# Performance work log

Hardware: AMD Instinct MI355X
Metric: run time of the kernel (lower is better)

## Reference

```python
import jax, jax.numpy as jnp
import numpy as np

B, N, BQ, BK = 2, 2048, 32, 128
NB = N // BQ
CS, CZ, CH, H, PQK, PV = 384, 128, 16, 12, 4, 8
INF, EPS = 1e5, 1e-8
CONCAT = CZ // 4 + CH + PV * 4  # per-head concat feature dim


def _ln(x, g, b):
    m = jnp.mean(x, -1, keepdims=True)
    v = jnp.mean((x - m) ** 2, -1, keepdims=True)
    return (x - m) * jax.lax.rsqrt(v + 1e-5) * g + b


def _forward(s, z, trans, rots, s_mask, key_idx,
             ln_s_g, ln_s_b, ln_z_g, ln_z_b,
             Wq, Wk, Wv, Wqp, Wkvp, Wb, Wdz, head_weights, Wout):
    sN = _ln(s, ln_s_g, ln_s_b)                     # [B,N,CS]
    zN = _ln(z, ln_z_g, ln_z_b)                     # [B,NB,BQ,BK,CZ]
    q_in = sN.reshape(B, NB, BQ, CS)                # to_queries = block reshape
    k_in = sN[:, key_idx]                           # to_keys = gather [B,NB,BK,CS]
    q_t = trans.reshape(B, NB, BQ, 3)
    q_R = rots.reshape(B, NB, BQ, 3, 3)
    k_t = trans[:, key_idx]                         # [B,NB,BK,3]
    k_R = rots[:, key_idx]                          # [B,NB,BK,3,3]

    q = (q_in @ Wq).reshape(B, NB, BQ, H, CH)
    k = (k_in @ Wk).reshape(B, NB, BK, H, CH)
    v = (k_in @ Wv).reshape(B, NB, BK, H, CH)

    # query points: local -> global frame (R p + t)
    q_pts = (q_in @ Wqp).reshape(B, NB, BQ, H * PQK, 3)
    q_pts = jnp.einsum('bnqij,bnqpj->bnqpi', q_R, q_pts) + q_t[..., None, :]
    q_pts = q_pts.reshape(B, NB, BQ, H, PQK, 3)
    kv_pts = (k_in @ Wkvp).reshape(B, NB, BK, H * (PQK + PV), 3)
    kv_pts = jnp.einsum('bnkij,bnkpj->bnkpi', k_R, kv_pts) + k_t[..., None, :]
    kv_pts = kv_pts.reshape(B, NB, BK, H, PQK + PV, 3)
    k_pts, v_pts = kv_pts[..., :PQK, :], kv_pts[..., PQK:, :]

    bbias = zN @ Wb                                 # [B,NB,BQ,BK,H]
    a = jnp.einsum('bnqhc,bnkhc->bnqkh', q, k) * np.float32(np.sqrt(1.0 / (3 * CH)))
    a = a + np.float32(np.sqrt(1.0 / 3)) * bbias

    # point-distance bias (pts_cdist=True path)
    pt = -2.0 * jnp.einsum('bnqhpd,bnkhpd->bnqkh', q_pts, k_pts)
    qn = jnp.sum(q_pts ** 2, axis=(-1, -2))         # [B,NB,BQ,H]
    kn = jnp.sum(k_pts ** 2, axis=(-1, -2))         # [B,NB,BK,H]
    pt = pt + qn[..., None, :] + kn[..., None, :, :]
    hw = jax.nn.softplus(head_weights) * np.float32(np.sqrt(1.0 / (3 * (PQK * 9.0 / 2))))
    pt = pt * hw * (-0.5)
    a = a + pt

    q_mask = s_mask.reshape(B, NB, BQ)
    k_mask = s_mask[:, key_idx]                     # [B,NB,BK]
    am = q_mask[..., :, None] * k_mask[..., None, :]  # [B,NB,BQ,BK]
    a = a + (INF * (am - 1.0))[..., None]
    a = jnp.swapaxes(a, -1, -2)                     # [B,NB,BQ,H,BK]
    a = jax.nn.softmax(a, axis=-1)

    o = jnp.einsum('bnqhk,bnkhc->bnqhc', a, v).reshape(B, NB, BQ, H * CH)
    o_pt = jnp.einsum('bnqhk,bnkhvc->bnqhvc', a, v_pts)   # [B,NB,BQ,H,PV,3]
    # invert apply: R^T (p - t), back into the query local frame
    o_pt = jnp.einsum('bnqji,bnqhvj->bnqhvi', q_R, o_pt - q_t[..., None, None, :])
    o_pt_d = jnp.sqrt(jnp.sum(o_pt ** 2, -1) + EPS).reshape(B, NB, BQ, H * PV)
    o_pt_f = o_pt.reshape(B, NB, BQ, H * PV * 3)
    pair_z = zN @ Wdz                               # [B,NB,BQ,BK,CZ//4]
    o_pair = jnp.einsum('bnqhk,bnqkc->bnqhc', a, pair_z).reshape(B, NB, BQ, H * (CZ // 4))

    feats = jnp.concatenate([o, o_pt_f, o_pt_d, o_pair], -1)  # [B,NB,BQ,H*CONCAT]
    out = feats @ Wout
    return out.reshape(B, N, CS)


def setup_inputs() -> dict:
    key = jax.random.key(0)
    ks = jax.random.split(key, 16)
    def p(i, shape, scale):
        return jax.random.normal(ks[i], shape, jnp.float32) * scale
    s = p(0, (B, N, CS), 1.0)
    z = p(1, (B, NB, BQ, BK, CZ), 1.0)
    trans = p(2, (B, N, 3), 1.0)
    rots = p(3, (B, N, 3, 3), 1.0)
    s_mask = jnp.ones((B, N), jnp.float32)
    starts = np.clip(np.arange(NB) * BQ - (BK - BQ) // 2, 0, N - BK)
    key_idx = jnp.asarray(starts[:, None] + np.arange(BK)[None, :], jnp.int32)
    return dict(
        s=s, z=z, trans=trans, rots=rots, s_mask=s_mask, key_idx=key_idx,
        ln_s_g=jnp.ones((CS,), jnp.float32), ln_s_b=jnp.zeros((CS,), jnp.float32),
        ln_z_g=jnp.ones((CZ,), jnp.float32), ln_z_b=jnp.zeros((CZ,), jnp.float32),
        Wq=p(4, (CS, H * CH), CS ** -0.5), Wk=p(5, (CS, H * CH), CS ** -0.5),
        Wv=p(6, (CS, H * CH), CS ** -0.5),
        Wqp=p(7, (CS, H * PQK * 3), CS ** -0.5),
        Wkvp=p(8, (CS, H * (PQK + PV) * 3), CS ** -0.5),
        Wb=p(9, (CZ, H), CZ ** -0.5), Wdz=p(10, (CZ, CZ // 4), CZ ** -0.5),
        head_weights=p(11, (H,), 0.5),
        Wout=p(12, (H * CONCAT, CS), 0.02),
    )


def reference(s, z, trans, rots, s_mask, key_idx,
              ln_s_g, ln_s_b, ln_z_g, ln_z_b,
              Wq, Wk, Wv, Wqp, Wkvp, Wb, Wdz, head_weights, Wout):
    return _forward(s, z, trans, rots, s_mask, key_idx,
                    ln_s_g, ln_s_b, ln_z_g, ln_z_b,
                    Wq, Wk, Wv, Wqp, Wkvp, Wb, Wdz, head_weights, Wout)
```

## Files before the change

kernel.cpp:

```cpp
#include <hip/hip_runtime.h>
#include <hip/hip_bf16.h>


typedef unsigned int uint_t;
typedef unsigned short ushort_t;
__device__ __forceinline__ float b2f(const __hip_bfloat16 x) { return __bfloat162float(x); }
__device__ __forceinline__ __hip_bfloat16 f2b(float x) { return __float2bfloat16(x); }
__device__ __forceinline__ ushort_t f2bu(float x) {
  __hip_bfloat16 h = __float2bfloat16(x);
  return *(ushort_t*)&h;
}
__device__ __forceinline__ float b2fu(ushort_t u) {
  union { uint_t i; float f; } c; c.i = ((uint_t)u) << 16; return c.f;
}
__device__ __forceinline__ uint_t pack2(float a, float b) {
  return (uint_t)f2bu(a) | ((uint_t)f2bu(b) << 16);
}
typedef __attribute__((ext_vector_type(8))) short short8x;
typedef __attribute__((ext_vector_type(4))) float floatx4;

__global__ __launch_bounds__(256) void k_ln(
    const float* __restrict__ s, const float* __restrict__ g_s,
    const float* __restrict__ b_s, float* __restrict__ sN,
    const float* __restrict__ g_z, const float* __restrict__ b_z,
    const float* __restrict__ Wb, const float* __restrict__ Wdz,
    ushort_t* __restrict__ Wt_g, float* __restrict__ uv_g)
{
  if (blockIdx.x >= 512) {
    const int tid = threadIdx.x;
    for (int e = tid; e < 48 * 128; e += 256) {
      int c = e >> 7, k = e & 127;
      float v = 0.f;
      if (c < 12)      v = g_z[k] * Wb[k * 12 + c];
      else if (c < 44) v = g_z[k] * Wdz[k * 32 + (c - 12)];
      Wt_g[e] = f2bu(v);
    }
    int c = tid >> 2, p = tid & 3;
    float us_ = 0.f, vs_ = 0.f;
    if (c < 44) {
      for (int k = p * 32; k < p * 32 + 32; k++) {
        float worig = (c < 12) ? Wb[k * 12 + c] : Wdz[k * 32 + (c - 12)];
        us_ += b2fu(f2bu(g_z[k] * worig));
        vs_ += b_z[k] * worig;
      }
    }
    us_ += __shfl_xor(us_, 1, 64); us_ += __shfl_xor(us_, 2, 64);
    vs_ += __shfl_xor(vs_, 1, 64); vs_ += __shfl_xor(vs_, 2, 64);
    if (p == 0 && c < 48) { uv_g[c] = us_; uv_g[48 + c] = vs_; }
    return;
  }
  const int tid = threadIdx.x;
  const int w = tid >> 6, l = tid & 63;
  #pragma unroll
  for (int ii = 0; ii < 2; ii++) {
    int row = blockIdx.x * 8 + w * 2 + ii;
    const float* sr = s + (size_t)row * 384;
    float x[6], s1 = 0.f, s2 = 0.f;
    #pragma unroll
    for (int j = 0; j < 6; j++) { x[j] = sr[l + j * 64]; s1 += x[j]; s2 += x[j] * x[j]; }
    #pragma unroll
    for (int m = 1; m < 64; m <<= 1) { s1 += __shfl_xor(s1, m, 64); s2 += __shfl_xor(s2, m, 64); }
    float mean = s1 * (1.f / 384.f);
    float var = s2 * (1.f / 384.f) - mean * mean;
    float rstd = rsqrtf(var + 1e-5f);
    float* dr = sN + (size_t)row * 384;
    #pragma unroll
    for (int j = 0; j < 6; j++) {
      int c = l + j * 64;
      dr[c] = (x[j] - mean) * rstd * g_s[c] + b_s[c];
    }
  }
}

__global__ __launch_bounds__(256) void k_zpg(
    const float* __restrict__ sN,
    const float* __restrict__ Wq, const float* __restrict__ Wk,
    const float* __restrict__ Wv, const float* __restrict__ Wqp,
    const float* __restrict__ Wkvp,
    float* __restrict__ proj,
    const float* __restrict__ z,
    const ushort_t* __restrict__ Wt_g, const float* __restrict__ uv_g,
    ushort_t* __restrict__ bbias_t, ushort_t* __restrict__ pzt)
{
  if (blockIdx.x < 1152) {
    __shared__ __align__(16) float sA[16][32];
    __shared__ __align__(16) float sB[16][128];
    const int tid = threadIdx.x;
    const int bid = blockIdx.x;
    const int mt = bid & 127;
    const int nt = bid >> 7;
    const int m0 = mt * 32, n0 = nt * 128;
    const int tm = tid >> 5, tn = tid & 31;

    const float* bsrc[2]; int bstride[2]; int bk[2];
    #pragma unroll
    for (int u = 0; u < 2; u++) {
      int idx = tid + u * 256;
      int k = idx >> 5, n4 = idx & 31;
      int col0 = n0 + n4 * 4;
      const float* p; int st;
      if (col0 < 192)      { p = Wq   + col0;         st = 192; }
      else if (col0 < 384) { p = Wk   + (col0 - 192); st = 192; }
      else if (col0 < 576) { p = Wv   + (col0 - 384); st = 192; }
      else if (col0 < 720) { p = Wqp  + (col0 - 576); st = 144; }
      else                 { p = Wkvp + (col0 - 720); st = 432; }
      bsrc[u] = p; bstride[u] = st; bk[u] = k;
    }
    const int am = tid >> 2, ak4 = tid & 3;

    float acc[4][4];
    #pragma unroll
    for (int i = 0; i < 4; i++)
      #pragma unroll
      for (int j = 0; j < 4; j++) acc[i][j] = 0.f;

    for (int k0 = 0; k0 < 384; k0 += 16) {
      #pragma unroll
      for (int u = 0; u < 2; u++) {
        float4 wv4 = *(const float4*)(bsrc[u] + (size_t)(k0 + bk[u]) * bstride[u]);
        *(float4*)&sB[bk[u]][(tid + u * 256 & 31) * 4] = wv4;
      }
      if (tid < 128) {
        float4 a4 = *(const float4*)(sN + (size_t)(m0 + am) * 384 + k0 + ak4 * 4);
        sA[ak4 * 4 + 0][am] = a4.x;
        sA[ak4 * 4 + 1][am] = a4.y;
        sA[ak4 * 4 + 2][am] = a4.z;
        sA[ak4 * 4 + 3][am] = a4.w;
      }
      __syncthreads();
      #pragma unroll
      for (int kk = 0; kk < 16; kk++) {
        float4 a4 = *(const float4*)&sA[kk][tm * 4];
        float4 b4 = *(const float4*)&sB[kk][tn * 4];
        const float* av = (const float*)&a4;
        const float* bv = (const float*)&b4;
        #pragma unroll
        for (int i = 0; i < 4; i++)
          #pragma unroll
          for (int j = 0; j < 4; j++) acc[i][j] += av[i] * bv[j];
      }
      __syncthreads();
    }
    #pragma unroll
    for (int i = 0; i < 4; i++)
      *(float4*)(proj + (size_t)(m0 + tm * 4 + i) * 1152 + n0 + tn * 4) = *(float4*)&acc[i][0];
  } else {
    const int tid = threadIdx.x;
    const int bid = blockIdx.x - 1152;
    const int w = tid >> 6, lane = tid & 63, quad = lane >> 4, r16 = lane & 15;
    const size_t row0 = (size_t)bid * 64;
    const int lrow = w * 16 + r16;
    const float* zr = z + (row0 + lrow) * 128;

    short8x bf[3][4];
    #pragma unroll
    for (int nt = 0; nt < 3; nt++)
      #pragma unroll
      for (int kk = 0; kk < 4; kk++)
        bf[nt][kk] = *(const short8x*)(Wt_g + (size_t)(nt * 16 + r16) * 128 + kk * 32 + quad * 8);

    union { short8x v; uint_t u[4]; } afu[4];
    float s1 = 0.f, s2 = 0.f;
    #pragma unroll
    for (int kk = 0; kk < 4; kk++) {
      float4 a = *(const float4*)(zr + kk * 32 + quad * 8);
      float4 b = *(const float4*)(zr + kk * 32 + quad * 8 + 4);
      s1 += a.x + a.y + a.z + a.w + b.x + b.y + b.z + b.w;
      s2 += a.x * a.x + a.y * a.y + a.z * a.z + a.w * a.w
          + b.x * b.x + b.y * b.y + b.z * b.z + b.w * b.w;
      afu[kk].u[0] = pack2(a.x, a.y);
      afu[kk].u[1] = pack2(a.z, a.w);
      afu[kk].u[2] = pack2(b.x, b.y);
      afu[kk].u[3] = pack2(b.z, b.w);
    }
    s1 += __shfl_xor(s1, 16, 64); s1 += __shfl_xor(s1, 32, 64);
    s2 += __shfl_xor(s2, 16, 64); s2 += __shfl_xor(s2, 32, 64);
    float mean = s1 * (1.f / 128.f);
    float rstd = rsqrtf(s2 * (1.f / 128.f) - mean * mean + 1e-5f);

    floatx4 acc[3] = { {0,0,0,0}, {0,0,0,0}, {0,0,0,0} };
    #pragma unroll
    for (int kk = 0; kk < 4; kk++)
      #pragma unroll
      for (int nt = 0; nt < 3; nt++)
        acc[nt] = __builtin_amdgcn_mfma_f32_16x16x32_bf16(afu[kk].v, bf[nt][kk], acc[nt], 0, 0, 0);

    float mr[4], rr[4];
    #pragma unroll
    for (int reg = 0; reg < 4; reg++) {
      int src = quad * 4 + reg;
      mr[reg] = __shfl(mean, src, 64);
      rr[reg] = __shfl(rstd, src, 64);
    }

    const int bp = bid >> 6;
    const int qk0 = (bid & 63) * 64;
    const int qloc = qk0 >> 7;
    const int kbase = (qk0 & 127) + w * 16 + quad * 4;
    #pragma unroll
    for (int nt = 0; nt < 3; nt++) {
      int c = nt * 16 + r16;
      if (c < 44) {
        float uc = uv_g[c], vc = uv_g[48 + c];
        float vals[4];
        #pragma unroll
        for (int reg = 0; reg < 4; reg++)
          vals[reg] = rr[reg] * acc[nt][reg] - mr[reg] * rr[reg] * uc + vc;
        uint2 pk = make_uint2(pack2(vals[0], vals[1]), pack2(vals[2], vals[3]));
        if (c < 12) {
          size_t el = (((size_t)(bp * 12 + c)) << 12) + qk0 + w * 16 + quad * 4;
          *(uint2*)(bbias_t + el) = pk;
        } else {
          size_t el = (((size_t)((bp * 32 + qloc) * 32 + (c - 12))) << 7) + kbase;
          *(uint2*)(pzt + el) = pk;
        }
      }
    }
  }
}

__global__ __launch_bounds__(256) void k_rot(
    const float* __restrict__ proj_g,
    const float* __restrict__ trans, const float* __restrict__ rots,
    float* __restrict__ posq, float* __restrict__ posk, float* __restrict__ posv,
    float* __restrict__ posqp, float* __restrict__ poskp, float* __restrict__ posvp,
    float* __restrict__ posqn, float* __restrict__ poskn)
{
  __shared__ __align__(16) float proj[8][1152];
  __shared__ float rt[8][12];
  const int tid = threadIdx.x;
  const int p0 = blockIdx.x * 8;

  for (int e = tid; e < 8 * 288; e += 256)
    ((float4*)&proj[0][0])[e] = ((const float4*)(proj_g + (size_t)p0 * 1152))[e];
  for (int e = tid; e < 8 * 12; e += 256) {
    int i = e / 12, c = e % 12;
    rt[i][c] = (c < 9) ? rots[(size_t)(p0 + i) * 9 + c]
                       : trans[(size_t)(p0 + i) * 3 + (c - 9)];
  }
  __syncthreads();

  for (int e = tid; e < 8 * 192; e += 256) {
    int i = e / 192, p = e % 192;
    float R0 = rt[i][0], R1 = rt[i][1], R2 = rt[i][2];
    float R3 = rt[i][3], R4 = rt[i][4], R5 = rt[i][5];
    float R6 = rt[i][6], R7 = rt[i][7], R8 = rt[i][8];
    float tx = rt[i][9], ty = rt[i][10], tz = rt[i][11];
    size_t pos = p0 + i;
    if (p < 48) {
      int base = 576 + p * 3;
      float v0 = proj[i][base], v1 = proj[i][base + 1], v2 = proj[i][base + 2];
      float o0 = R0 * v0 + R1 * v1 + R2 * v2 + tx;
      float o1 = R3 * v0 + R4 * v1 + R5 * v2 + ty;
      float o2 = R6 * v0 + R7 * v1 + R8 * v2 + tz;
      proj[i][base] = o0; proj[i][base + 1] = o1; proj[i][base + 2] = o2;
      posqp[pos * 144 + p * 3 + 0] = o0;
      posqp[pos * 144 + p * 3 + 1] = o1;
      posqp[pos * 144 + p * 3 + 2] = o2;
    } else {
      int p2 = p - 48;
      int base = 720 + p2 * 3;
      float v0 = proj[i][base], v1 = proj[i][base + 1], v2 = proj[i][base + 2];
      float o0 = R0 * v0 + R1 * v1 + R2 * v2 + tx;
      float o1 = R3 * v0 + R4 * v1 + R5 * v2 + ty;
      float o2 = R6 * v0 + R7 * v1 + R8 * v2 + tz;
      int h = p2 / 12, idx = p2 % 12;
      if (idx < 4) {
        proj[i][base] = o0; proj[i][base + 1] = o1; proj[i][base + 2] = o2;
        poskp[pos * 144 + h * 12 + idx * 3 + 0] = o0;
        poskp[pos * 144 + h * 12 + idx * 3 + 1] = o1;
        poskp[pos * 144 + h * 12 + idx * 3 + 2] = o2;
      } else {
        posvp[pos * 288 + h * 24 + (idx - 4) * 3 + 0] = o0;
        posvp[pos * 288 + h * 24 + (idx - 4) * 3 + 1] = o1;
        posvp[pos * 288 + h * 24 + (idx - 4) * 3 + 2] = o2;
      }
    }
  }
  __syncthreads();

  for (int e = tid; e < 96; e += 256) {
    int i = e / 12, h = e % 12;
    size_t pos = p0 + i;
    float qs = 0.f, ks = 0.f;
    #pragma unroll
    for (int u = 0; u < 12; u++) {
      float a_ = proj[i][576 + h * 12 + u];
      qs += a_ * a_;
      float c_ = proj[i][720 + h * 36 + u];
      ks += c_ * c_;
    }
    posqn[pos * 12 + h] = qs;
    poskn[pos * 12 + h] = ks;
  }
  for (int e = tid; e < 8 * 576; e += 256) {
    int i = e / 576, c = e % 576;
    size_t pos = p0 + i;
    float v = proj[i][c];
    if (c < 192)      posq[pos * 192 + c]         = v;
    else if (c < 384) posk[pos * 192 + (c - 192)] = v;
    else              posv[pos * 192 + (c - 384)] = v;
  }
}

__global__ __launch_bounds__(256) void k_attn(
    const float* __restrict__ posq, const float* __restrict__ posk,
    const float* __restrict__ posv, const float* __restrict__ posqp,
    const float* __restrict__ poskp, const float* __restrict__ posvp,
    const float* __restrict__ posqn, const float* __restrict__ poskn,
    const ushort_t* __restrict__ bbias_t,
    const float* __restrict__ s_mask, const int* __restrict__ key_idx,
    const float* __restrict__ trans, const float* __restrict__ rots,
    const float* __restrict__ head_w,
    float* __restrict__ feats, ushort_t* __restrict__ P_ws)
{
  __shared__ __align__(16) ushort_t sK[2 * 128 * 40];
  __shared__ __align__(16) ushort_t sV[2 * 48 * 136];
  __shared__ __align__(16) ushort_t sQ[2 * 32 * 40];
  __shared__ __align__(16) ushort_t sP[64 * 136];
  __shared__ float sOpt[64 * 25];
  __shared__ float rt[32][12];
  __shared__ float kn_l[2][128];
  __shared__ float qn_l[2][32];
  __shared__ float kmask[128];
  __shared__ float qmask[32];
  __shared__ int   kidx[128];
  __shared__ float hwe2[2];

  const int tid = threadIdx.x;
  const int bid = blockIdx.x;
  const int b = bid / 384;
  const int rem = bid % 384;
  const int nb = rem / 6;
  const int hp = rem % 6;
  const int h0 = hp * 2;
  const int rowbase = b * 2048 + nb * 32;

  if (tid < 128) kidx[tid] = key_idx[nb * 128 + tid];
  if (tid < 2) hwe2[tid] = -0.5f * 0.13608276348795434f * log1pf(expf(head_w[h0 + tid]));
  __syncthreads();

  if (tid < 128) kmask[tid] = s_mask[b * 2048 + kidx[tid]];
  if (tid < 32) qmask[tid] = s_mask[rowbase + tid];
  for (int e = tid; e < 384; e += 256) {
    int i = e / 12, c = e % 12;
    rt[i][c] = (c < 9) ? rots[(size_t)(rowbase + i) * 9 + c]
                       : trans[(size_t)(rowbase + i) * 3 + (c - 9)];
  }

  {
    int hh = tid >> 7, k = tid & 127, h = h0 + hh;
    int gk = b * 2048 + kidx[k];
    kn_l[hh][k] = poskn[(size_t)gk * 12 + h];
    float sq = 0.14433756729740643f;
    float sp = -2.f * hwe2[hh];
    const float* kr = posk + (size_t)gk * 192 + h * 16;
    #pragma unroll
    for (int c4 = 0; c4 < 4; c4++) {
      float4 v4 = *(const float4*)(kr + c4 * 4);
      uint2 pk = make_uint2(pack2(sq * v4.x, sq * v4.y), pack2(sq * v4.z, sq * v4.w));
      *(uint2*)&sK[(hh * 128 + k) * 40 + c4 * 4] = pk;
    }
    const float* kpr = poskp + (size_t)gk * 144 + h * 12;
    #pragma unroll
    for (int c4 = 0; c4 < 3; c4++) {
      float4 v4 = *(const float4*)(kpr + c4 * 4);
      uint2 pk = make_uint2(pack2(sp * v4.x, sp * v4.y), pack2(sp * v4.z, sp * v4.w));
      *(uint2*)&sK[(hh * 128 + k) * 40 + 16 + c4 * 4] = pk;
    }
    *(uint2*)&sK[(hh * 128 + k) * 40 + 28] = make_uint2(0u, 0u);
  }
  {
    int hh = tid >> 7, t7 = tid & 127, h = h0 + hh;
    int k2 = t7 >> 1, cg = t7 & 1, kk0 = k2 * 2;
    int ga = b * 2048 + kidx[kk0], gb = b * 2048 + kidx[kk0 + 1];
    if (cg == 0) {
      const float* A_ = posv + (size_t)ga * 192 + h * 16;
      const float* B_ = posv + (size_t)gb * 192 + h * 16;
      #pragma unroll
      for (int c4 = 0; c4 < 4; c4++) {
        float4 a4 = *(const float4*)(A_ + c4 * 4);
        float4 b4 = *(const float4*)(B_ + c4 * 4);
        #pragma unroll
        for (int j = 0; j < 4; j++)
          *(uint_t*)&sV[(hh * 48 + c4 * 4 + j) * 136 + kk0] =
              pack2(((const float*)&a4)[j], ((const float*)&b4)[j]);
      }
    } else {
      const float* A_ = posvp + (size_t)ga * 288 + h * 24;
      const float* B_ = posvp + (size_t)gb * 288 + h * 24;
      #pragma unroll
      for (int c4 = 0; c4 < 6; c4++) {
        float4 a4 = *(const float4*)(A_ + c4 * 4);
        float4 b4 = *(const float4*)(B_ + c4 * 4);
        #pragma unroll
        for (int j = 0; j < 4; j++)
          *(uint_t*)&sV[(hh * 48 + 16 + c4 * 4 + j) * 136 + kk0] =
              pack2(((const float*)&a4)[j], ((const float*)&b4)[j]);
      }
      #pragma unroll
      for (int j = 0; j < 8; j++)
        *(uint_t*)&sV[(hh * 48 + 40 + j) * 136 + kk0] = 0u;
    }
  }
  if (tid < 64) {
    int hh = tid >> 5, q = tid & 31, h = h0 + hh;
    qn_l[hh][q] = posqn[(size_t)(rowbase + q) * 12 + h];
    const float* qr = posq + (size_t)(rowbase + q) * 192 + h * 16;
    #pragma unroll
    for (int c4 = 0; c4 < 4; c4++) {
      float4 v4 = *(const float4*)(qr + c4 * 4);
      uint2 pk = make_uint2(pack2(v4.x, v4.y), pack2(v4.z, v4.w));
      *(uint2*)&sQ[(hh * 32 + q) * 40 + c4 * 4] = pk;
    }
    const float* qpr = posqp + (size_t)(rowbase + q) * 144 + h * 12;
    #pragma unroll
    for (int c4 = 0; c4 < 3; c4++) {
      float4 v4 = *(const float4*)(qpr + c4 * 4);
      uint2 pk = make_uint2(pack2(v4.x, v4.y), pack2(v4.z, v4.w));
      *(uint2*)&sQ[(hh * 32 + q) * 40 + 16 + c4 * 4] = pk;
    }
    *(uint2*)&sQ[(hh * 32 + q) * 40 + 28] = make_uint2(0u, 0u);
  }
  __syncthreads();

  const int w = tid >> 6, lane = tid & 63, quad = lane >> 4, r16 = lane & 15;
  const int hh = w >> 1, q0 = (w & 1) * 16;
  const int h = h0 + hh;
  const float hwe = hwe2[hh];

  short8x af = *(const short8x*)&sQ[(hh * 32 + q0 + r16) * 40 + quad * 8];
  floatx4 acc[8];
  #pragma unroll
  for (int nt = 0; nt < 8; nt++) {
    floatx4 z4 = {0.f, 0.f, 0.f, 0.f};
    short8x bf = *(const short8x*)&sK[(hh * 128 + nt * 16 + r16) * 40 + quad * 8];
    acc[nt] = __builtin_amdgcn_mfma_f32_16x16x32_bf16(af, bf, z4, 0, 0, 0);
  }

  const ushort_t* bb = bbias_t + (((size_t)((b * 64 + nb) * 12 + h)) << 12);
  float lg[8][4];
  #pragma unroll
  for (int nt = 0; nt < 8; nt++)
    #pragma unroll
    for (int reg = 0; reg < 4; reg++) {
      int qa = q0 + quad * 4 + reg;
      lg[nt][reg] = b2fu(bb[qa * 128 + nt * 16 + r16]);
    }
  float qnv[4], qmv[4];
  #pragma unroll
  for (int reg = 0; reg < 4; reg++) {
    int qa = q0 + quad * 4 + reg;
    qnv[reg] = qn_l[hh][qa]; qmv[reg] = qmask[qa];
  }
  #pragma unroll
  for (int nt = 0; nt < 8; nt++) {
    int col = nt * 16 + r16;
    float knv = kn_l[hh][col], kmv = kmask[col];
    #pragma unroll
    for (int reg = 0; reg < 4; reg++)
      lg[nt][reg] = acc[nt][reg] + 0.5773502691896258f * lg[nt][reg]
                  + hwe * (qnv[reg] + knv) + 100000.f * (qmv[reg] * kmv - 1.f);
  }
  float mx[4], sm[4];
  #pragma unroll
  for (int reg = 0; reg < 4; reg++) {
    float m = lg[0][reg];
    #pragma unroll
    for (int nt = 1; nt < 8; nt++) m = fmaxf(m, lg[nt][reg]);
    #pragma unroll
    for (int d = 1; d < 16; d <<= 1) m = fmaxf(m, __shfl_xor(m, d, 64));
    mx[reg] = m; sm[reg] = 0.f;
  }
  #pragma unroll
  for (int nt = 0; nt < 8; nt++)
    #pragma unroll
    for (int reg = 0; reg < 4; reg++) {
      float e = __expf(lg[nt][reg] - mx[reg]);
      lg[nt][reg] = e; sm[reg] += e;
    }
  #pragma unroll
  for (int reg = 0; reg < 4; reg++) {
    float s = sm[reg];
    #pragma unroll
    for (int d = 1; d < 16; d <<= 1) s += __shfl_xor(s, d, 64);
    sm[reg] = 1.f / s;
  }
  #pragma unroll
  for (int nt = 0; nt < 8; nt++)
    #pragma unroll
    for (int reg = 0; reg < 4; reg++) {
      int row = quad * 4 + reg;
      sP[(w * 16 + row) * 136 + nt * 16 + r16] = f2bu(lg[nt][reg] * sm[reg]);
    }
  short8x afp[4];
  #pragma unroll
  for (int kk = 0; kk < 4; kk++)
    afp[kk] = *(const short8x*)&sP[(w * 16 + r16) * 136 + kk * 32 + quad * 8];
  floatx4 o0 = {0.f,0.f,0.f,0.f}, o1 = {0.f,0.f,0.f,0.f}, o2 = {0.f,0.f,0.f,0.f};
  #pragma unroll
  for (int kk = 0; kk < 4; kk++) {
    short8x bv0 = *(const short8x*)&sV[(hh * 48 +  0 + r16) * 136 + kk * 32 + quad * 8];
    short8x bv1 = *(const short8x*)&sV[(hh * 48 + 16 + r16) * 136 + kk * 32 + quad * 8];
    short8x bv2 = *(const short8x*)&sV[(hh * 48 + 32 + r16) * 136 + kk * 32 + quad * 8];
    o0 = __builtin_amdgcn_mfma_f32_16x16x32_bf16(afp[kk], bv0, o0, 0, 0, 0);
    o1 = __builtin_amdgcn_mfma_f32_16x16x32_bf16(afp[kk], bv1, o1, 0, 0, 0);
    o2 = __builtin_amdgcn_mfma_f32_16x16x32_bf16(afp[kk], bv2, o2, 0, 0, 0);
  }
  #pragma unroll
  for (int reg = 0; reg < 4; reg++) {
    int qa = q0 + quad * 4 + reg;
    feats[(size_t)(rowbase + qa) * 960 + h * 16 + r16] = o0[reg];
  }
  #pragma unroll
  for (int reg = 0; reg < 4; reg++) {
    int row = quad * 4 + reg;
    sOpt[(w * 16 + row) * 25 + r16] = o1[reg];
    if (r16 < 8) sOpt[(w * 16 + row) * 25 + 16 + r16] = o2[reg];
  }
  for (int e2 = lane; e2 < 128; e2 += 64) {
    int ql = e2 >> 3, v = e2 & 7;
    int qa = q0 + ql;
    float u0 = sOpt[(w * 16 + ql) * 25 + v * 3 + 0] - rt[qa][9];
    float u1 = sOpt[(w * 16 + ql) * 25 + v * 3 + 1] - rt[qa][10];
    float u2 = sOpt[(w * 16 + ql) * 25 + v * 3 + 2] - rt[qa][11];
    float w0 = rt[qa][0] * u0 + rt[qa][3] * u1 + rt[qa][6] * u2;
    float w1 = rt[qa][1] * u0 + rt[qa][4] * u1 + rt[qa][7] * u2;
    float w2 = rt[qa][2] * u0 + rt[qa][5] * u1 + rt[qa][8] * u2;
    size_t fb = (size_t)(rowbase + qa) * 960;
    feats[fb + 192 + h * 24 + v * 3 + 0] = w0;
    feats[fb + 192 + h * 24 + v * 3 + 1] = w1;
    feats[fb + 192 + h * 24 + v * 3 + 2] = w2;
    feats[fb + 480 + h * 8 + v] = sqrtf(w0 * w0 + w1 * w1 + w2 * w2 + 1e-8f);
  }
  {
    uint_t* Pg = (uint_t*)P_ws;
    size_t pb2 = (((size_t)((b * 64 + nb) * 12 + h)) << 12) >> 1;
    #pragma unroll
    for (int ql = 0; ql < 16; ql++) {
      uint_t pv = *(const uint_t*)&sP[(w * 16 + ql) * 136 + 2 * lane];
      Pg[pb2 + (size_t)(q0 + ql) * 64 + lane] = pv;
    }
  }
}

__global__ __launch_bounds__(256) void k_opair(
    const ushort_t* __restrict__ P_ws, const ushort_t* __restrict__ pzt,
    float* __restrict__ feats)
{
  __shared__ __align__(16) ushort_t pzl[4 * 32 * 136];
  const int tid = threadIdx.x;
  const int w = tid >> 6, lane = tid & 63, quad = lane >> 4, r16 = lane & 15;
  const int bid = blockIdx.x;
  const int b = bid >> 9, rem = bid & 511, nb = rem >> 3, qg = rem & 7;
  const int q = qg * 4 + w;
  const int rowbase = b * 2048 + nb * 32;

  const uint_t* src = (const uint_t*)pzt + ((((size_t)((b * 64 + nb) * 32 + q)) << 12) >> 1);
  #pragma unroll
  for (int c = 0; c < 32; c++) {
    uint_t v = src[c * 64 + lane];
    *(uint_t*)&pzl[(w * 32 + c) * 136 + 2 * lane] = v;
  }
  const ushort_t* Pp = P_ws + ((size_t)(b * 64 + nb) * 12) * 4096
                            + (size_t)r16 * 4096 + (size_t)q * 128;
  short8x af[4];
  #pragma unroll
  for (int kk = 0; kk < 4; kk++)
    af[kk] = *(const short8x*)(Pp + kk * 32 + quad * 8);

  floatx4 acc[2] = { {0.f,0.f,0.f,0.f}, {0.f,0.f,0.f,0.f} };
  #pragma unroll
  for (int kk = 0; kk < 4; kk++) {
    #pragma unroll
    for (int nt = 0; nt < 2; nt++) {
      short8x bf = *(const short8x*)&pzl[(w * 32 + nt * 16 + r16) * 136 + kk * 32 + quad * 8];
      acc[nt] = __builtin_amdgcn_mfma_f32_16x16x32_bf16(af[kk], bf, acc[nt], 0, 0, 0);
    }
  }
  #pragma unroll
  for (int nt = 0; nt < 2; nt++)
    #pragma unroll
    for (int reg = 0; reg < 4; reg++) {
      int hrow = quad * 4 + reg;
      if (hrow < 12)
        feats[(size_t)(rowbase + q) * 960 + 576 + hrow * 32 + nt * 16 + r16] = acc[nt][reg];
    }
}

__global__ __launch_bounds__(256) void k_out(
    const float* __restrict__ feats, const float* __restrict__ Wout,
    float* __restrict__ out)
{
  __shared__ __align__(16) float frow[16][960];
  const int tid = threadIdx.x;
  const int p0 = blockIdx.x * 16;
  for (int e = tid; e < 16 * 240; e += 256) {
    int i = e / 240, cc = e % 240;
    ((float4*)&frow[i][0])[cc] = ((const float4*)&feats[(size_t)(p0 + i) * 960])[cc];
  }
  __syncthreads();
  const int w = tid >> 6, l = tid & 63;
  const int c0 = l * 6;
  float acc[4][6];
  #pragma unroll
  for (int i = 0; i < 4; i++)
    #pragma unroll
    for (int j = 0; j < 6; j++) acc[i][j] = 0.f;

  for (int ch = 0; ch < 240; ch++) {
    float4 f4[4];
    #pragma unroll
    for (int i = 0; i < 4; i++) f4[i] = *(const float4*)&frow[w * 4 + i][ch * 4];
    #pragma unroll
    for (int rr = 0; rr < 4; rr++) {
      int r = ch * 4 + rr;
      const float2* wp = (const float2*)(Wout + (size_t)r * 384 + c0);
      float2 w0 = wp[0], w1 = wp[1], w2 = wp[2];
      float wv[6] = { w0.x, w0.y, w1.x, w1.y, w2.x, w2.y };
      #pragma unroll
      for (int i = 0; i < 4; i++) {
        float fv = ((const float*)&f4[i])[rr];
        #pragma unroll
        for (int j = 0; j < 6; j++) acc[i][j] += fv * wv[j];
      }
    }
  }
  #pragma unroll
  for (int i = 0; i < 4; i++)
    #pragma unroll
    for (int j = 0; j < 6; j++)
      out[(size_t)(p0 + w * 4 + i) * 384 + c0 + j] = acc[i][j];
}

extern "C" void kernel_launch(void* const* d_in, const int* in_sizes, int n_in,
                              void* d_out, int out_size, void* d_ws, size_t ws_size,
                              hipStream_t stream) {
  const float* s      = (const float*)d_in[0];
  const float* z      = (const float*)d_in[1];
  const float* trans  = (const float*)d_in[2];
  const float* rots   = (const float*)d_in[3];
  const float* s_mask = (const float*)d_in[4];
  const int*   key_idx= (const int*)d_in[5];
  const float* ln_s_g = (const float*)d_in[6];
  const float* ln_s_b = (const float*)d_in[7];
  const float* ln_z_g = (const float*)d_in[8];
  const float* ln_z_b = (const float*)d_in[9];
  const float* Wq     = (const float*)d_in[10];
  const float* Wk     = (const float*)d_in[11];
  const float* Wv     = (const float*)d_in[12];
  const float* Wqp    = (const float*)d_in[13];
  const float* Wkvp   = (const float*)d_in[14];
  const float* Wb     = (const float*)d_in[15];
  const float* Wdz    = (const float*)d_in[16];
  const float* head_w = (const float*)d_in[17];
  const float* Wout   = (const float*)d_in[18];

  char* wsb = (char*)d_ws;
  float* posq  = (float*)(wsb + 0);
  float* posk  = (float*)(wsb + 3145728);
  float* posv  = (float*)(wsb + 6291456);
  float* posqp = (float*)(wsb + 9437184);
  float* poskp = (float*)(wsb + 11796480);
  float* posvp = (float*)(wsb + 14155776);
  float* posqn = (float*)(wsb + 18874368);
  float* poskn = (float*)(wsb + 19070976);
  float* feats = (float*)(wsb + 19267584);
  float* sN    = (float*)(wsb + 19267584);
  float* proj  = (float*)(wsb + 34996224);
  ushort_t* bbias_t = (ushort_t*)(wsb + 53870592);
  ushort_t* pzt     = (ushort_t*)(wsb + 66453504);
  ushort_t* P_ws    = (ushort_t*)(wsb + 100007936);
  ushort_t* Wt_ws   = (ushort_t*)(wsb + 112590848);
  float*    uv_ws   = (float*)(wsb + 112603136);

  k_ln<<<513, 256, 0, stream>>>(s, ln_s_g, ln_s_b, sN,
                                ln_z_g, ln_z_b, Wb, Wdz, Wt_ws, uv_ws);
  k_zpg<<<9344, 256, 0, stream>>>(sN, Wq, Wk, Wv, Wqp, Wkvp, proj,
                                  z, Wt_ws, uv_ws, bbias_t, pzt);
  k_rot<<<512, 256, 0, stream>>>(proj, trans, rots,
                                 posq, posk, posv, posqp, poskp, posvp, posqn, poskn);
  k_attn<<<768, 256, 0, stream>>>(posq, posk, posv, posqp, poskp, posvp, posqn, poskn,
                                  bbias_t, s_mask, key_idx, trans, rots, head_w,
                                  feats, P_ws);
  k_opair<<<1024, 256, 0, stream>>>(P_ws, pzt, feats);
  k_out<<<256, 256, 0, stream>>>(feats, Wout, (float*)d_out);
}
```

Before: 654.4 us.

## Move output projection to bf16x3 MFMA with transposed split weights

The final output projection moves from scalar FP32 FMAs to MFMA 16x16x32 bf16 instructions. Near-FP32 accuracy is kept by splitting both operands into hi and lo bf16 parts and summing three products. Extra blocks in the layer-norm kernel pre-transpose and split Wout into hi/lo bf16 buffers in the workspace, and k_out now uses 512 threads and converts the feats rows in shared memory. This adds a small preprocessing cost and slightly changes numerics, since the lo*lo term is dropped.

```diff
diff --git a/kernel.cpp b/kernel.cpp
--- a/kernel.cpp
+++ b/kernel.cpp
@@ -24,9 +24,24 @@
     const float* __restrict__ b_s, float* __restrict__ sN,
     const float* __restrict__ g_z, const float* __restrict__ b_z,
     const float* __restrict__ Wb, const float* __restrict__ Wdz,
-    ushort_t* __restrict__ Wt_g, float* __restrict__ uv_g)
+    ushort_t* __restrict__ Wt_g, float* __restrict__ uv_g,
+    const float* __restrict__ Wout,
+    ushort_t* __restrict__ woT_hi, ushort_t* __restrict__ woT_lo)
 {
-  if (blockIdx.x >= 512) {
+  if (blockIdx.x >= 513) {
+    const int tid = threadIdx.x;
+    const int c = (blockIdx.x - 513) * 4 + (tid >> 6);
+    const int lane = tid & 63;
+    for (int k0 = 0; k0 < 960; k0 += 64) {
+      int k = k0 + lane;
+      float x = Wout[(size_t)k * 384 + c];
+      ushort_t hu = f2bu(x);
+      woT_hi[(size_t)c * 960 + k] = hu;
+      woT_lo[(size_t)c * 960 + k] = f2bu(x - b2fu(hu));
+    }
+    return;
+  }
+  if (blockIdx.x == 512) {
     const int tid = threadIdx.x;
     for (int e = tid; e < 48 * 128; e += 256) {
       int c = e >> 7, k = e & 127;
@@ -588,49 +603,54 @@
     }
 }
 
-__global__ __launch_bounds__(256) void k_out(
-    const float* __restrict__ feats, const float* __restrict__ Wout,
+__global__ __launch_bounds__(512) void k_out(
+    const float* __restrict__ feats,
+    const ushort_t* __restrict__ woT_hi, const ushort_t* __restrict__ woT_lo,
     float* __restrict__ out)
 {
-  __shared__ __align__(16) float frow[16][960];
+  __shared__ __align__(16) ushort_t hiA[16 * 968];
+  __shared__ __align__(16) ushort_t loA[16 * 968];
   const int tid = threadIdx.x;
   const int p0 = blockIdx.x * 16;
-  for (int e = tid; e < 16 * 240; e += 256) {
-    int i = e / 240, cc = e % 240;
-    ((float4*)&frow[i][0])[cc] = ((const float4*)&feats[(size_t)(p0 + i) * 960])[cc];
+
+  for (int e = tid; e < 16 * 240; e += 512) {
+    int i = e / 240, c4 = e % 240;
+    float4 v = ((const float4*)&feats[(size_t)(p0 + i) * 960])[c4];
+    ushort_t h0 = f2bu(v.x), h1 = f2bu(v.y), h2 = f2bu(v.z), h3 = f2bu(v.w);
+    uint2 hp = make_uint2((uint_t)h0 | ((uint_t)h1 << 16), (uint_t)h2 | ((uint_t)h3 << 16));
+    uint2 lp = make_uint2(pack2(v.x - b2fu(h0), v.y - b2fu(h1)),
+                          pack2(v.z - b2fu(h2), v.w - b2fu(h3)));
+    *(uint2*)&hiA[i * 968 + c4 * 4] = hp;
+    *(uint2*)&loA[i * 968 + c4 * 4] = lp;
   }
   __syncthreads();
-  const int w = tid >> 6, l = tid & 63;
-  const int c0 = l * 6;
-  float acc[4][6];
-  #pragma unroll
-  for (int i = 0; i < 4; i++)
-    #pragma unroll
-    for (int j = 0; j < 6; j++) acc[i][j] = 0.f;
-
-  for (int ch = 0; ch < 240; ch++) {
-    float4 f4[4];
-    #pragma unroll
-    for (int i = 0; i < 4; i++) f4[i] = *(const float4*)&frow[w * 4 + i][ch * 4];
-    #pragma unroll
-    for (int rr = 0; rr < 4; rr++) {
-      int r = ch * 4 + rr;
-      const float2* wp = (const float2*)(Wout + (size_t)r * 384 + c0);
-      float2 w0 = wp[0], w1 = wp[1], w2 = wp[2];
-      float wv[6] = { w0.x, w0.y, w1.x, w1.y, w2.x, w2.y };
-      #pragma unroll
-      for (int i = 0; i < 4; i++) {
-        float fv = ((const float*)&f4[i])[rr];
-        #pragma unroll
-        for (int j = 0; j < 6; j++) acc[i][j] += fv * wv[j];
-      }
-    }
-  }
-  #pragma unroll
-  for (int i = 0; i < 4; i++)
-    #pragma unroll
-    for (int j = 0; j < 6; j++)
-      out[(size_t)(p0 + w * 4 + i) * 384 + c0 + j] = acc[i][j];
+
+  const int wv = tid >> 6, lane = tid & 63, quad = lane >> 4, r16 = lane & 15;
+  const int n0 = wv * 48;
+  floatx4 acc[3] = { {0.f,0.f,0.f,0.f}, {0.f,0.f,0.f,0.f}, {0.f,0.f,0.f,0.f} };
+
+  #pragma unroll 2
+  for (int ks = 0; ks < 30; ks++) {
+    int k0 = ks * 32;
+    short8x ah = *(const short8x*)&hiA[r16 * 968 + k0 + quad * 8];
+    short8x al = *(const short8x*)&loA[r16 * 968 + k0 + quad * 8];
+    #pragma unroll
+    for (int nt = 0; nt < 3; nt++) {
+      size_t bo = (size_t)(n0 + nt * 16 + r16) * 960 + k0 + quad * 8;
+      short8x bh = *(const short8x*)(woT_hi + bo);
+      short8x bl = *(const short8x*)(woT_lo + bo);
+      acc[nt] = __builtin_amdgcn_mfma_f32_16x16x32_bf16(ah, bh, acc[nt], 0, 0, 0);
+      acc[nt] = __builtin_amdgcn_mfma_f32_16x16x32_bf16(al, bh, acc[nt], 0, 0, 0);
+      acc[nt] = __builtin_amdgcn_mfma_f32_16x16x32_bf16(ah, bl, acc[nt], 0, 0, 0);
+    }
+  }
+  #pragma unroll
+  for (int nt = 0; nt < 3; nt++)
+    #pragma unroll
+    for (int reg = 0; reg < 4; reg++) {
+      int row = quad * 4 + reg;
+      out[(size_t)(p0 + row) * 384 + n0 + nt * 16 + r16] = acc[nt][reg];
+    }
 }
 
 extern "C" void kernel_launch(void* const* d_in, const int* in_sizes, int n_in,
@@ -673,9 +693,12 @@
   ushort_t* P_ws    = (ushort_t*)(wsb + 100007936);
   ushort_t* Wt_ws   = (ushort_t*)(wsb + 112590848);
   float*    uv_ws   = (float*)(wsb + 112603136);
-
-  k_ln<<<513, 256, 0, stream>>>(s, ln_s_g, ln_s_b, sN,
-                                ln_z_g, ln_z_b, Wb, Wdz, Wt_ws, uv_ws);
+  ushort_t* woT_hi  = (ushort_t*)(wsb + 112603520);
+  ushort_t* woT_lo  = (ushort_t*)(wsb + 113340800);
+
+  k_ln<<<609, 256, 0, stream>>>(s, ln_s_g, ln_s_b, sN,
+                                ln_z_g, ln_z_b, Wb, Wdz, Wt_ws, uv_ws,
+                                Wout, woT_hi, woT_lo);
   k_zpg<<<9344, 256, 0, stream>>>(sN, Wq, Wk, Wv, Wqp, Wkvp, proj,
                                   z, Wt_ws, uv_ws, bbias_t, pzt);
   k_rot<<<512, 256, 0, stream>>>(proj, trans, rots,
@@ -684,5 +707,5 @@
                                   bbias_t, s_mask, key_idx, trans, rots, head_w,
                                   feats, P_ws);
   k_opair<<<1024, 256, 0, stream>>>(P_ws, pzt, feats);
-  k_out<<<256, 256, 0, stream>>>(feats, Wout, (float*)d_out);
-}
+  k_out<<<256, 512, 0, stream>>>(feats, woT_hi, woT_lo, (float*)d_out);
+}
```

After: 562.9 us. -14.0%, faster.
